# Kernel tuning notes

Measured on AMD Instinct MI355X. Metric: run time of the kernel, lower is better.

## Reference

```python
import jax, jax.numpy as jnp
import numpy as np

# ----- module constants (from init_kwargs) -----
N = 1024          # Np = [N, N]
NZ = 16           # number of slices (O.shape[3])
NA = 0.65         # objective NA
WL = 0.5          # wavelength (um)
PS = 6.5          # camera pixel size (um)
MAG = 20.0        # magnification
PS_EFF = PS / MAG
DZ = 10.0 * PS / MAG                 # slice spacing (code overwrites wl/na**2)
KAPPA = 2.0 * np.pi * DZ / WL        # imag part of self.k
K = np.complex64(1j * KAPPA)         # self.k as a complex scalar


def _grids():
    c = (np.arange(N) - N // 2) * PS_EFF
    xx, yy = np.meshgrid(c, c)                       # spatial grids
    f = (np.arange(N) - N // 2) / (PS_EFF * N)
    uxx, uyy = np.meshgrid(f, f)                     # frequency grids
    return xx, yy, uxx, uyy

_XX, _YY, _UXX, _UYY = _grids()
_URR = _UXX ** 2 + _UYY ** 2
_PC = (_URR < (NA / WL) ** 2).astype(np.float64)     # centered pupil


def _fresnel(dz):
    # genFrensel: band-limited angular-spectrum kernel, stored in fft order
    kz = np.sqrt(np.maximum(_PC * ((1.0 / WL) ** 2 - _URR), 0.0))
    kern = _PC * np.exp(1j * 2.0 * np.pi * dz * kz)
    return jnp.asarray(np.fft.fftshift(kern).astype(np.complex64))

PUPIL = jnp.asarray(np.fft.fftshift(_PC).astype(np.complex64))   # fft order
PROPKERN = _fresnel(DZ)
PROPKERN_FOCUS = _fresnel(-DZ * (NZ - 1) / 2.0)
XX = jnp.asarray(_XX, jnp.float32)
YY = jnp.asarray(_YY, jnp.float32)


def _prop(u, kern):
    # torch.fft / torch.ifft pair == unnormalized fft2 / normalized ifft2
    return jnp.fft.ifft2(jnp.fft.fft2(u) * kern)


def _plane_wave(na_illum):
    dfx = 1.0 / (PS_EFF * N)
    tilt = jnp.round((na_illum / WL) / dfx) * dfx    # snap tilt to freq grid
    phase = 2.0 * np.pi * (tilt[0] * XX + tilt[1] * YY)
    return jnp.exp(1j * phase)                        # complex64


def _ms_grad(O, intensity, na_illum):
    """Faithful translation of Multislice.grad. O: [N,N,NZ] complex64."""
    T = jnp.exp(K * O)                                # per-slice transmittance
    u = _plane_wave(na_illum)
    # forward multislice propagation
    for zz in range(NZ):
        u = T[..., zz] * u
        if zz < NZ - 1:
            u = _prop(u, PROPKERN)
    # refocus to stack center, apply pupil
    u_ref = _prop(u, PROPKERN_FOCUS)
    u_pup = _prop(u_ref, PUPIL)
    # amplitude-replacement residual
    abs_field = jnp.abs(u_pup)
    comp = jnp.sqrt(intensity) * u_pup / abs_field
    residual = u_pup - comp
    # back-propagate residual
    u_bp = _prop(residual, jnp.conj(PUPIL))
    u_bp = _prop(u_bp, jnp.conj(PROPKERN_FOCUS))
    # reverse slice loop accumulating per-slice gradient
    grads = [None] * NZ
    for zz in range(NZ - 1, -1, -1):
        grads[zz] = u_bp * jnp.conj(u) * jnp.conj(T[..., zz]) * np.conj(K)
        if zz > 0:
            u_bp = _prop(u_bp * jnp.conj(T[..., zz]), jnp.conj(PROPKERN))
            u = _prop(u, jnp.conj(PROPKERN))
            u = u / T[..., zz - 1]
    return jnp.stack(grads, axis=-1)                  # [N,N,NZ] complex


def setup_inputs() -> dict:
    key = jax.random.key(0)
    k1, k2, k3 = jax.random.split(key, 3)
    # small-valued object so exp(i*KAPPA*O) stays bounded (KAPPA ~ 40.8)
    x = jax.random.normal(k1, (N, N, 2, NZ), jnp.float32) * 0.01
    meas = jax.random.uniform(k2, (N, N), jnp.float32) + 0.1
    na_illum = jax.random.uniform(k3, (2,), jnp.float32) * 0.2
    alpha = jnp.full((1,), 0.01, jnp.float32)
    return {"x": x, "meas": meas, "na_illum": na_illum, "alpha": alpha}


def reference(x, meas, na_illum, alpha):
    # forward: x + step(x) = x - alpha * grad(x, meas, na_illum)
    O = x[..., 0, :] + 1j * x[..., 1, :]              # [N,N,NZ] complex64
    g = _ms_grad(O, meas, na_illum)
    out = O - alpha[0] * g
    return jnp.stack((out.real, out.imag), axis=2)    # back to [N,N,2,NZ]
```

## Files before the change

### kernel.cpp

```cpp
#include <hip/hip_runtime.h>
#include <math.h>


#define NN (1024*1024)
#define KAPPA 40.840704496667314f
#define TWO_PI_F 6.2831853071795865f
#define DFX_D 0.0030048076923076925
#define RRCUT 187177
#define F(i) ((i) + ((i)>>4))

#define JT 0
#define JT_WP 1
#define JRESID 3

__device__ __forceinline__ float2 cmulf(float2 a, float2 b){
    return make_float2(a.x*b.x - a.y*b.y, a.x*b.y + a.y*b.x);
}
__device__ __forceinline__ float2 cmulcj(float2 a, float2 b){
    return make_float2(a.x*b.x + a.y*b.y, a.y*b.x - a.x*b.y);
}
__device__ __forceinline__ float2 f2add(float2 a, float2 b){ return make_float2(a.x+b.x, a.y+b.y); }
__device__ __forceinline__ float2 f2sub(float2 a, float2 b){ return make_float2(a.x-b.x, a.y-b.y); }

__device__ __forceinline__ void fill_tw(float2* tw, int tid){
    #pragma unroll
    for (int k = tid; k < 512; k += 256){
        float s, c; sincosf(-(float)k * (TWO_PI_F/1024.0f), &s, &c);
        tw[k] = make_float2(c, s);
    }
}

__device__ __forceinline__ void dif_ph1(float2 r[8], const float2* tw, int lane){
    float2 a, d;
    #pragma unroll
    for (int k=0;k<4;++k){
        a=r[k]; d=f2sub(r[k],r[k+4]);
        r[k]=f2add(a,r[k+4]);
        r[k+4]=cmulf(d, tw[lane+128*k]);
    }
    float2 w20 = tw[lane<<1], w21 = tw[(lane+128)<<1];
    a=r[0]; d=f2sub(r[0],r[2]); r[0]=f2add(a,r[2]); r[2]=cmulf(d,w20);
    a=r[1]; d=f2sub(r[1],r[3]); r[1]=f2add(a,r[3]); r[3]=cmulf(d,w21);
    a=r[4]; d=f2sub(r[4],r[6]); r[4]=f2add(a,r[6]); r[6]=cmulf(d,w20);
    a=r[5]; d=f2sub(r[5],r[7]); r[5]=f2add(a,r[7]); r[7]=cmulf(d,w21);
    float2 w3 = tw[lane<<2];
    a=r[0]; d=f2sub(r[0],r[1]); r[0]=f2add(a,r[1]); r[1]=cmulf(d,w3);
    a=r[2]; d=f2sub(r[2],r[3]); r[2]=f2add(a,r[3]); r[3]=cmulf(d,w3);
    a=r[4]; d=f2sub(r[4],r[5]); r[4]=f2add(a,r[5]); r[5]=cmulf(d,w3);
    a=r[6]; d=f2sub(r[6],r[7]); r[6]=f2add(a,r[7]); r[7]=cmulf(d,w3);
}
__device__ __forceinline__ void dit_ph1(float2 r[8], const float2* tw, int lane){
    float2 a, b;
    float2 w3 = tw[lane<<2];
    a=r[0]; b=cmulcj(r[1],w3); r[0]=f2add(a,b); r[1]=f2sub(a,b);
    a=r[2]; b=cmulcj(r[3],w3); r[2]=f2add(a,b); r[3]=f2sub(a,b);
    a=r[4]; b=cmulcj(r[5],w3); r[4]=f2add(a,b); r[5]=f2sub(a,b);
    a=r[6]; b=cmulcj(r[7],w3); r[6]=f2add(a,b); r[7]=f2sub(a,b);
    float2 w20 = tw[lane<<1], w21 = tw[(lane+128)<<1];
    a=r[0]; b=cmulcj(r[2],w20); r[0]=f2add(a,b); r[2]=f2sub(a,b);
    a=r[1]; b=cmulcj(r[3],w21); r[1]=f2add(a,b); r[3]=f2sub(a,b);
    a=r[4]; b=cmulcj(r[6],w20); r[4]=f2add(a,b); r[6]=f2sub(a,b);
    a=r[5]; b=cmulcj(r[7],w21); r[5]=f2add(a,b); r[7]=f2sub(a,b);
    #pragma unroll
    for (int k=0;k<4;++k){
        a=r[k]; b=cmulcj(r[k+4], tw[lane+128*k]);
        r[k]=f2add(a,b); r[k+4]=f2sub(a,b);
    }
}
__device__ __forceinline__ void dif_ph2(float2 r[8], const float2* tw, int m0){
    float2 a, d;
    #pragma unroll
    for (int k=0;k<4;++k){
        a=r[k]; d=f2sub(r[k],r[k+4]);
        r[k]=f2add(a,r[k+4]);
        r[k+4]=cmulf(d, tw[(m0+16*k)<<3]);
    }
    float2 w40 = tw[m0<<4], w41 = tw[(m0+16)<<4];
    a=r[0]; d=f2sub(r[0],r[2]); r[0]=f2add(a,r[2]); r[2]=cmulf(d,w40);
    a=r[1]; d=f2sub(r[1],r[3]); r[1]=f2add(a,r[3]); r[3]=cmulf(d,w41);
    a=r[4]; d=f2sub(r[4],r[6]); r[4]=f2add(a,r[6]); r[6]=cmulf(d,w40);
    a=r[5]; d=f2sub(r[5],r[7]); r[5]=f2add(a,r[7]); r[7]=cmulf(d,w41);
    float2 w5 = tw[m0<<5];
    a=r[0]; d=f2sub(r[0],r[1]); r[0]=f2add(a,r[1]); r[1]=cmulf(d,w5);
    a=r[2]; d=f2sub(r[2],r[3]); r[2]=f2add(a,r[3]); r[3]=cmulf(d,w5);
    a=r[4]; d=f2sub(r[4],r[5]); r[4]=f2add(a,r[5]); r[5]=cmulf(d,w5);
    a=r[6]; d=f2sub(r[6],r[7]); r[6]=f2add(a,r[7]); r[7]=cmulf(d,w5);
}
__device__ __forceinline__ void dit_ph2(float2 r[8], const float2* tw, int m0){
    float2 a, b;
    float2 w5 = tw[m0<<5];
    a=r[0]; b=cmulcj(r[1],w5); r[0]=f2add(a,b); r[1]=f2sub(a,b);
    a=r[2]; b=cmulcj(r[3],w5); r[2]=f2add(a,b); r[3]=f2sub(a,b);
    a=r[4]; b=cmulcj(r[5],w5); r[4]=f2add(a,b); r[5]=f2sub(a,b);
    a=r[6]; b=cmulcj(r[7],w5); r[6]=f2add(a,b); r[7]=f2sub(a,b);
    float2 w40 = tw[m0<<4], w41 = tw[(m0+16)<<4];
    a=r[0]; b=cmulcj(r[2],w40); r[0]=f2add(a,b); r[2]=f2sub(a,b);
    a=r[1]; b=cmulcj(r[3],w41); r[1]=f2add(a,b); r[3]=f2sub(a,b);
    a=r[4]; b=cmulcj(r[6],w40); r[4]=f2add(a,b); r[6]=f2sub(a,b);
    a=r[5]; b=cmulcj(r[7],w41); r[5]=f2add(a,b); r[7]=f2sub(a,b);
    #pragma unroll
    for (int k=0;k<4;++k){
        a=r[k]; b=cmulcj(r[k+4], tw[(m0+16*k)<<3]);
        r[k]=f2add(a,b); r[k+4]=f2sub(a,b);
    }
}
__device__ __forceinline__ void dif_reg(float2 r[8]){
    const float C = 0.70710678118654752f;
    float2 a,d;
    a=r[0]; d=f2sub(r[0],r[4]); r[0]=f2add(a,r[4]); r[4]=d;
    a=r[1]; d=f2sub(r[1],r[5]); r[1]=f2add(a,r[5]); r[5]=make_float2(C*(d.x+d.y), C*(d.y-d.x));
    a=r[2]; d=f2sub(r[2],r[6]); r[2]=f2add(a,r[6]); r[6]=make_float2(d.y, -d.x);
    a=r[3]; d=f2sub(r[3],r[7]); r[3]=f2add(a,r[7]); r[7]=make_float2(C*(d.y-d.x), -C*(d.x+d.y));
    a=r[0]; r[0]=f2add(a,r[2]); r[2]=f2sub(a,r[2]);
    a=r[1]; d=f2sub(r[1],r[3]); r[1]=f2add(a,r[3]); r[3]=make_float2(d.y,-d.x);
    a=r[4]; r[4]=f2add(a,r[6]); r[6]=f2sub(a,r[6]);
    a=r[5]; d=f2sub(r[5],r[7]); r[5]=f2add(a,r[7]); r[7]=make_float2(d.y,-d.x);
    a=r[0]; r[0]=f2add(a,r[1]); r[1]=f2sub(a,r[1]);
    a=r[2]; r[2]=f2add(a,r[3]); r[3]=f2sub(a,r[3]);
    a=r[4]; r[4]=f2add(a,r[5]); r[5]=f2sub(a,r[5]);
    a=r[6]; r[6]=f2add(a,r[7]); r[7]=f2sub(a,r[7]);
}
__device__ __forceinline__ void dit_reg(float2 r[8]){
    const float C = 0.70710678118654752f;
    float2 a,b,t;
    a=r[0]; r[0]=f2add(a,r[1]); r[1]=f2sub(a,r[1]);
    a=r[2]; r[2]=f2add(a,r[3]); r[3]=f2sub(a,r[3]);
    a=r[4]; r[4]=f2add(a,r[5]); r[5]=f2sub(a,r[5]);
    a=r[6]; r[6]=f2add(a,r[7]); r[7]=f2sub(a,r[7]);
    a=r[0]; r[0]=f2add(a,r[2]); r[2]=f2sub(a,r[2]);
    a=r[1]; t=r[3]; b=make_float2(-t.y, t.x); r[1]=f2add(a,b); r[3]=f2sub(a,b);
    a=r[4]; r[4]=f2add(a,r[6]); r[6]=f2sub(a,r[6]);
    a=r[5]; t=r[7]; b=make_float2(-t.y, t.x); r[5]=f2add(a,b); r[7]=f2sub(a,b);
    a=r[0]; r[0]=f2add(a,r[4]); r[4]=f2sub(a,r[4]);
    a=r[1]; t=r[5]; b=make_float2(C*(t.x-t.y), C*(t.x+t.y)); r[1]=f2add(a,b); r[5]=f2sub(a,b);
    a=r[2]; t=r[6]; b=make_float2(-t.y, t.x); r[2]=f2add(a,b); r[6]=f2sub(a,b);
    a=r[3]; t=r[7]; b=make_float2(-C*(t.x+t.y), C*(t.x-t.y)); r[3]=f2add(a,b); r[7]=f2sub(a,b);
}

__device__ __forceinline__ void st128l(float2* L, int ro, int lane, const float2 r[8]){
    #pragma unroll
    for (int k=0;k<8;++k) L[F(ro + lane + 128*k)] = r[k];
}
__device__ __forceinline__ void ld128l(const float2* L, int ro, int lane, float2 r[8]){
    #pragma unroll
    for (int k=0;k<8;++k) r[k] = L[F(ro + lane + 128*k)];
}
__device__ __forceinline__ void st16l(float2* L, int ro, int lane, const float2 r[8]){
    int b = lane>>4, m0 = lane&15, q = ro + 128*b + m0;
    #pragma unroll
    for (int k=0;k<8;++k) L[F(q + 16*k)] = r[k];
}
__device__ __forceinline__ void ld16l(const float2* L, int ro, int lane, float2 r[8]){
    int b = lane>>4, m0 = lane&15, q = ro + 128*b + m0;
    #pragma unroll
    for (int k=0;k<8;++k) r[k] = L[F(q + 16*k)];
}
__device__ __forceinline__ void st8l(float2* L, int ro, int lane, const float2 r[8]){
    int q = ro + 8*lane;
    #pragma unroll
    for (int i=0;i<8;++i) L[F(q + i)] = r[i];
}
__device__ __forceinline__ void ldfold_dif(const float2* L, int ro, int lane,
                                           const float2* tw, float2 r[8]){
    int rr = lane>>1, sub = lane&1, q = ro + 16*rr;
    #pragma unroll
    for (int i=0;i<8;++i){
        float2 x = L[F(q + i)];
        float2 y = L[F(q + 8 + i)];
        r[i] = sub ? cmulf(f2sub(x,y), tw[i<<6]) : f2add(x,y);
    }
}
__device__ __forceinline__ void ldfold_dit(const float2* L, int ro, int lane,
                                           const float2* tw, float2 r[8]){
    int b = lane>>4, m0 = lane&15, m0s = m0&7;
    float2 w = tw[m0s<<6];
    int q = ro + 128*b + m0s;
    #pragma unroll
    for (int k=0;k<8;++k){
        float2 x = L[F(q + 16*k)];
        float2 y = L[F(q + 16*k + 8)];
        float2 bb = cmulcj(y, w);
        r[k] = (m0 < 8) ? f2add(x,bb) : f2sub(x,bb);
    }
}
__device__ __forceinline__ void load8g(const float2* src, int lane, float2 r[8]){
    const float4* s4 = (const float4*)src + lane*4;
    #pragma unroll
    for (int m=0;m<4;++m){
        float4 v = s4[m];
        r[2*m]   = make_float2(v.x, v.y);
        r[2*m+1] = make_float2(v.z, v.w);
    }
}
__device__ __forceinline__ void twrite2(const float2* L, int tid, float2* dst,
                                        int r0, float s){
    #pragma unroll
    for (int k=0;k<4;++k){
        int c = tid + (k<<8);
        float2 a0 = L[F(c)], a1 = L[F(1024+c)];
        ((float4*)(dst + ((size_t)c<<10) + r0))[0] =
            make_float4(a0.x*s, a0.y*s, a1.x*s, a1.y*s);
    }
}

__global__ void __launch_bounds__(256) k_head(float2* __restrict__ dst,
                                              const float2* __restrict__ T0,
                                              const float* __restrict__ nail){
    __shared__ float2 A[2176], B[2176], tw[512];
    const int tid = threadIdx.x;
    fill_tw(tw, tid);
    const int row = tid>>7, lane = tid&127, ro = row<<10, m0 = lane&15;
    const int r0 = blockIdx.x*2;
    const size_t gbase = ((size_t)(r0+row))<<10;
    float dfx = (float)DFX_D;
    float t0 = rintf(nail[0]*2.0f/dfx)*dfx;
    float t1 = rintf(nail[1]*2.0f/dfx)*dfx;
    float yv = (float)((r0+row) - 512) * 0.325f;
    float2 r[8];
    #pragma unroll
    for (int k=0;k<8;++k){
        int col = lane + 128*k;
        float2 tv = T0[gbase + col];
        float xv = (float)(col - 512) * 0.325f;
        float s0, c0; sincosf(TWO_PI_F*(t0*xv + t1*yv), &s0, &c0);
        r[k] = cmulf(make_float2(c0,s0), tv);
    }
    __syncthreads();
    dif_ph1(r, tw, lane);
    st128l(A, ro, lane, r); __syncthreads();
    ld16l(A, ro, lane, r); dif_ph2(r, tw, m0);
    st16l(B, ro, lane, r); __syncthreads();
    ldfold_dif(B, ro, lane, tw, r); dif_reg(r);
    st8l(A, ro, lane, r); __syncthreads();
    twrite2(A, tid, dst, r0, 1.0f);
}

__global__ void __launch_bounds__(256) k_pass2(
    const float2* __restrict__ srcA, float2* __restrict__ dstA,
    const float2* __restrict__ srcB, float2* __restrict__ dstB,
    double zscale, float sg)
{
    __shared__ float2 A[2176], B[2176], tw[512];
    const int tid = threadIdx.x;
    fill_tw(tw, tid);
    const int row = tid>>7, lane = tid&127, ro = row<<10, m0 = lane&15;
    int bid = blockIdx.x;
    const float2* src = srcA; float2* dst = dstA;
    if (srcB != nullptr && bid >= 512){ src = srcB; dst = dstB; bid -= 512; }
    const int r0 = bid*2;
    const int jrow = r0 + row;
    const float2* srcR = src + (((size_t)r0)<<10) + ro;
    float2 r[8];
    #pragma unroll
    for (int k=0;k<8;++k) r[k] = srcR[lane + 128*k];
    __syncthreads();
    dif_ph1(r, tw, lane);
    st128l(A, ro, lane, r); __syncthreads();
    ld16l(A, ro, lane, r); dif_ph2(r, tw, m0);
    st16l(B, ro, lane, r); __syncthreads();
    ldfold_dif(B, ro, lane, tw, r); dif_reg(r);
    {
        int bb = __brev((unsigned)jrow) >> 22;
        int rb = bb - (bb >= 512 ? 1024 : 0);
        int rb2 = rb*rb;
        #pragma unroll
        for (int i=0;i<8;++i){
            int aa = __brev((unsigned)(8*lane+i)) >> 22;
            int ra = aa - (aa >= 512 ? 1024 : 0);
            int rr = ra*ra + rb2;
            if (rr <= RRCUT){
                double urr = (double)rr * (DFX_D*DFX_D);
                double kz = sqrt(4.0 - urr);
                double t = zscale * kz;
                float fp = (float)(t - floor(t));
                float s, c; sincosf(TWO_PI_F*fp, &s, &c);
                r[i] = cmulf(r[i], make_float2(c, sg*s));
            } else {
                r[i] = make_float2(0.f, 0.f);
            }
        }
    }
    dit_reg(r);
    st8l(A, ro, lane, r); __syncthreads();
    ldfold_dit(A, ro, lane, tw, r); dit_ph2(r, tw, m0);
    st16l(B, ro, lane, r); __syncthreads();
    ld128l(B, ro, lane, r); dit_ph1(r, tw, lane);
    st128l(A, ro, lane, r); __syncthreads();
    twrite2(A, tid, dst, r0, 1.0f/1024.0f);
}

__global__ void __launch_bounds__(256) k_junc(
    const float2* __restrict__ src, float2* __restrict__ dst,
    const float2* __restrict__ Tz, float2* __restrict__ wp,
    const float* __restrict__ meas, int mode)
{
    __shared__ float2 A[2176], B[2176], tw[512];
    const int tid = threadIdx.x;
    fill_tw(tw, tid);
    const int row = tid>>7, lane = tid&127, ro = row<<10, m0 = lane&15;
    const int r0 = blockIdx.x*2;
    const size_t gbase = ((size_t)(r0+row))<<10;
    const float S = 1.0f/1024.0f;
    float2 r[8];
    load8g(src + (((size_t)r0)<<10) + ro, lane, r);
    float2 pre[8];
    if (mode == JT || mode == JT_WP){
        #pragma unroll
        for (int k=0;k<8;++k) pre[k] = Tz[gbase + lane + 128*k];
    } else if (mode == JRESID){
        #pragma unroll
        for (int k=0;k<8;++k) pre[k].x = meas[gbase + lane + 128*k];
    }
    dit_reg(r);
    st8l(A, ro, lane, r); __syncthreads();
    ldfold_dit(A, ro, lane, tw, r); dit_ph2(r, tw, m0);
    st16l(B, ro, lane, r); __syncthreads();
    ld128l(B, ro, lane, r); dit_ph1(r, tw, lane);
    #pragma unroll
    for (int k=0;k<8;++k){
        size_t g = gbase + lane + 128*k;
        float2 v = make_float2(S*r[k].x, S*r[k].y);
        if (mode == JT || mode == JT_WP){
            v = cmulf(v, pre[k]);
            if (mode == JT_WP) wp[g] = v;
        } else if (mode == JRESID){
            float m = pre[k].x;
            float aamp = fmaxf(sqrtf(v.x*v.x + v.y*v.y), 1e-30f);
            float f = 1.0f - sqrtf(m)/aamp;
            v.x *= f; v.y *= f;
        }
        r[k] = v;
    }
    dif_ph1(r, tw, lane);
    st128l(A, ro, lane, r); __syncthreads();
    ld16l(A, ro, lane, r); dif_ph2(r, tw, m0);
    st16l(B, ro, lane, r); __syncthreads();
    ldfold_dif(B, ro, lane, tw, r); dif_reg(r);
    st8l(A, ro, lane, r); __syncthreads();
    twrite2(A, tid, dst, r0, 1.0f);
}

__global__ void __launch_bounds__(256) k_rev(
    const float2* __restrict__ srcU, float2* __restrict__ dstU,
    const float2* __restrict__ srcB, float2* __restrict__ dstB,
    float2* __restrict__ Tz, int headU)
{
    __shared__ float2 A[2176], B[2176], tw[512];
    const int tid = threadIdx.x;
    fill_tw(tw, tid);
    const int row = tid>>7, lane = tid&127, ro = row<<10, m0 = lane&15;
    const int r0 = blockIdx.x*2;
    const size_t gbase = ((size_t)(r0+row))<<10;
    const float S = 1.0f/1024.0f;
    float2 u[8], Tg[8], bb[8], r[8];
    if (!headU){
        load8g(srcU + (((size_t)r0)<<10) + ro, lane, u);
    } else {
        const float2* srcR = srcU + (((size_t)r0)<<10) + ro;
        #pragma unroll
        for (int k=0;k<8;++k) u[k] = srcR[lane + 128*k];
    }
    #pragma unroll
    for (int k=0;k<8;++k) Tg[k] = Tz[gbase + lane + 128*k];
    load8g(srcB + (((size_t)r0)<<10) + ro, lane, bb);
    if (!headU){
        dit_reg(u);
        st8l(A, ro, lane, u); __syncthreads();
        ldfold_dit(A, ro, lane, tw, u); dit_ph2(u, tw, m0);
        st16l(B, ro, lane, u); __syncthreads();
        ld128l(B, ro, lane, u); dit_ph1(u, tw, lane);
        #pragma unroll
        for (int k=0;k<8;++k){ u[k].x *= S; u[k].y *= S; }
    } else {
        __syncthreads();
    }
    #pragma unroll
    for (int k=0;k<8;++k){
        if (headU) r[k] = u[k];
        else {
            float inv = 1.0f/(Tg[k].x*Tg[k].x + Tg[k].y*Tg[k].y);
            float2 wc = cmulcj(u[k], Tg[k]);
            r[k] = make_float2(wc.x*inv, wc.y*inv);
        }
    }
    dif_ph1(r, tw, lane);
    st128l(A, ro, lane, r); __syncthreads();
    ld16l(A, ro, lane, r); dif_ph2(r, tw, m0);
    st16l(B, ro, lane, r); __syncthreads();
    ldfold_dif(B, ro, lane, tw, r); dif_reg(r);
    st8l(A, ro, lane, r); __syncthreads();
    twrite2(A, tid, dstU, r0, 1.0f);
    dit_reg(bb);
    st8l(B, ro, lane, bb); __syncthreads();
    ldfold_dit(B, ro, lane, tw, r); dit_ph2(r, tw, m0);
    st16l(A, ro, lane, r); __syncthreads();
    ld128l(A, ro, lane, r); dit_ph1(r, tw, lane);
    #pragma unroll
    for (int k=0;k<8;++k){
        float2 b = make_float2(S*r[k].x, S*r[k].y);
        float2 q = headU ? cmulcj(cmulcj(b, u[k]), Tg[k]) : cmulcj(b, u[k]);
        Tz[gbase + lane + 128*k] = make_float2(KAPPA*q.y, -KAPPA*q.x);
        r[k] = cmulcj(b, Tg[k]);
    }
    dif_ph1(r, tw, lane);
    st128l(B, ro, lane, r); __syncthreads();
    ld16l(B, ro, lane, r); dif_ph2(r, tw, m0);
    st16l(A, ro, lane, r); __syncthreads();
    ldfold_dif(A, ro, lane, tw, r); dif_reg(r);
    st8l(B, ro, lane, r); __syncthreads();
    twrite2(B, tid, dstB, r0, 1.0f);
}

__global__ void __launch_bounds__(256) k_tail(
    const float2* __restrict__ srcU, const float2* __restrict__ srcB,
    float2* __restrict__ G0)
{
    __shared__ float2 A[2176], B[2176], tw[512];
    const int tid = threadIdx.x;
    fill_tw(tw, tid);
    const int row = tid>>7, lane = tid&127, ro = row<<10, m0 = lane&15;
    const int r0 = blockIdx.x*2;
    const size_t gbase = ((size_t)(r0+row))<<10;
    const float S = 1.0f/1024.0f;
    float2 u[8], r[8];
    load8g(srcU + (((size_t)r0)<<10) + ro, lane, u);
    load8g(srcB + (((size_t)r0)<<10) + ro, lane, r);
    dit_reg(u);
    st8l(A, ro, lane, u); __syncthreads();
    ldfold_dit(A, ro, lane, tw, u); dit_ph2(u, tw, m0);
    st16l(B, ro, lane, u); __syncthreads();
    ld128l(B, ro, lane, u); dit_ph1(u, tw, lane);
    dit_reg(r);
    st8l(A, ro, lane, r); __syncthreads();
    ldfold_dit(A, ro, lane, tw, r); dit_ph2(r, tw, m0);
    st16l(B, ro, lane, r); __syncthreads();
    ld128l(B, ro, lane, r); dit_ph1(r, tw, lane);
    #pragma unroll
    for (int k=0;k<8;++k){
        float2 b = make_float2(S*r[k].x, S*r[k].y);
        float2 w = make_float2(S*u[k].x, S*u[k].y);
        float2 q = cmulcj(b, w);
        G0[gbase + lane + 128*k] = make_float2(KAPPA*q.y, -KAPPA*q.x);
    }
}

__global__ void __launch_bounds__(256) k_T(const float4* __restrict__ x,
                                           float2* __restrict__ T){
    int idx = blockIdx.x*256 + threadIdx.x;
    int pp = idx >> 2;
    int q  = idx & 3;
    int p0 = pp*2;
    float4 vr0 = x[(size_t)p0*8 + q];
    float4 vi0 = x[(size_t)p0*8 + 4 + q];
    float4 vr1 = x[(size_t)(p0+1)*8 + q];
    float4 vi1 = x[(size_t)(p0+1)*8 + 4 + q];
    const float* fr0 = (const float*)&vr0;
    const float* fi0 = (const float*)&vi0;
    const float* fr1 = (const float*)&vr1;
    const float* fi1 = (const float*)&vi1;
    #pragma unroll
    for (int j=0;j<4;++j){
        int z = 4*q + j;
        float a0 = __expf(-KAPPA*fi0[j]);
        float s0, c0; __sincosf(KAPPA*fr0[j], &s0, &c0);
        float a1 = __expf(-KAPPA*fi1[j]);
        float s1, c1; __sincosf(KAPPA*fr1[j], &s1, &c1);
        ((float4*)(T + (size_t)z*NN + p0))[0] = make_float4(a0*c0, a0*s0, a1*c1, a1*s1);
    }
}

__global__ void __launch_bounds__(256) k_merge(const float4* __restrict__ x,
                                               const float2* __restrict__ G,
                                               const float* __restrict__ alpha,
                                               float4* __restrict__ out){
    int idx = blockIdx.x*256 + threadIdx.x;
    int p = idx >> 2, q = idx & 3;
    float al = alpha[0];
    float4 xr = x[(size_t)p*8 + q];
    float4 xi = x[(size_t)p*8 + 4 + q];
    float2 g[4];
    #pragma unroll
    for (int j=0;j<4;++j) g[j] = G[(size_t)(4*q+j)*NN + p];
    out[(size_t)p*8 + q]     = make_float4(xr.x - al*g[0].x, xr.y - al*g[1].x,
                                           xr.z - al*g[2].x, xr.w - al*g[3].x);
    out[(size_t)p*8 + 4 + q] = make_float4(xi.x - al*g[0].y, xi.y - al*g[1].y,
                                           xi.z - al*g[2].y, xi.w - al*g[3].y);
}

extern "C" void kernel_launch(void* const* d_in, const int* in_sizes, int n_in,
                              void* d_out, int out_size, void* d_ws, size_t ws_size,
                              hipStream_t stream)
{
    const float* x     = (const float*)d_in[0];
    const float* meas  = (const float*)d_in[1];
    const float* nail  = (const float*)d_in[2];
    const float* alpha = (const float*)d_in[3];

    if (ws_size < (size_t)21*NN*sizeof(float2)) return;

    float2* W   = (float2*)d_ws;
    float2* T   = W;
    float2* U0  = W + (size_t)16*NN;
    float2* TAB = W + (size_t)17*NN;
    float2* TBB = W + (size_t)18*NN;
    float2* TAU = W + (size_t)19*NN;
    float2* TBU = W + (size_t)20*NN;

    const double ZP = 3.25;
    const double ZF = -24.375;

    k_T <<<8192, 256, 0, stream>>>((const float4*)x, T);

    auto P2f = [&](double zs, float sg){
        k_pass2<<<512, 256, 0, stream>>>(TAB, TBB, nullptr, nullptr, zs, sg);
    };

    k_head<<<512, 256, 0, stream>>>(TAB, T, nail);
    P2f(ZP, 1.0f);
    for (int z = 1; z <= 14; ++z){
        k_junc<<<512, 256, 0, stream>>>(TBB, TAB, T + (size_t)z*NN, nullptr, nullptr, JT);
        P2f(ZP, 1.0f);
    }
    k_junc<<<512, 256, 0, stream>>>(TBB, TAB, T + (size_t)15*NN, U0, nullptr, JT_WP);
    P2f(ZF, 1.0f);
    k_junc<<<512, 256, 0, stream>>>(TBB, TAB, nullptr, nullptr, meas, JRESID);
    P2f(ZF, -1.0f);

    for (int zz = 15; zz >= 1; --zz){
        k_rev<<<512, 256, 0, stream>>>(zz == 15 ? U0 : TBU, TAU, TBB, TAB,
                                       T + (size_t)zz*NN, zz == 15 ? 1 : 0);
        k_pass2<<<1024, 256, 0, stream>>>(TAB, TBB, TAU, TBU, ZP, -1.0f);
    }
    k_tail<<<512, 256, 0, stream>>>(TBU, TBB, T);

    k_merge<<<16384, 256, 0, stream>>>((const float4*)x, T, alpha, (float4*)d_out);
}
```

Before: 1.421 ms.

## Switch row FFTs to radix-4 with 512 threads and fewer shared buffers

```diff
diff --git a/kernel.cpp b/kernel.cpp
--- a/kernel.cpp
+++ b/kernel.cpp
@@ -8,6 +8,7 @@
 #define DFX_D 0.0030048076923076925
 #define RRCUT 187177
 #define F(i) ((i) + ((i)>>4))
+#define NTW 768
 
 #define JT 0
 #define JT_WP 1
@@ -22,251 +23,197 @@
 __device__ __forceinline__ float2 f2add(float2 a, float2 b){ return make_float2(a.x+b.x, a.y+b.y); }
 __device__ __forceinline__ float2 f2sub(float2 a, float2 b){ return make_float2(a.x-b.x, a.y-b.y); }
 
-__device__ __forceinline__ void fill_tw(float2* tw, int tid){
-    #pragma unroll
-    for (int k = tid; k < 512; k += 256){
+__device__ __forceinline__ void fill_tw768(float2* tw, int tid){
+    for (int k = tid; k < NTW; k += 512){
         float s, c; sincosf(-(float)k * (TWO_PI_F/1024.0f), &s, &c);
         tw[k] = make_float2(c, s);
     }
 }
 
-__device__ __forceinline__ void dif_ph1(float2 r[8], const float2* tw, int lane){
-    float2 a, d;
-    #pragma unroll
-    for (int k=0;k<4;++k){
-        a=r[k]; d=f2sub(r[k],r[k+4]);
-        r[k]=f2add(a,r[k+4]);
-        r[k+4]=cmulf(d, tw[lane+128*k]);
-    }
-    float2 w20 = tw[lane<<1], w21 = tw[(lane+128)<<1];
-    a=r[0]; d=f2sub(r[0],r[2]); r[0]=f2add(a,r[2]); r[2]=cmulf(d,w20);
-    a=r[1]; d=f2sub(r[1],r[3]); r[1]=f2add(a,r[3]); r[3]=cmulf(d,w21);
-    a=r[4]; d=f2sub(r[4],r[6]); r[4]=f2add(a,r[6]); r[6]=cmulf(d,w20);
-    a=r[5]; d=f2sub(r[5],r[7]); r[5]=f2add(a,r[7]); r[7]=cmulf(d,w21);
-    float2 w3 = tw[lane<<2];
-    a=r[0]; d=f2sub(r[0],r[1]); r[0]=f2add(a,r[1]); r[1]=cmulf(d,w3);
-    a=r[2]; d=f2sub(r[2],r[3]); r[2]=f2add(a,r[3]); r[3]=cmulf(d,w3);
-    a=r[4]; d=f2sub(r[4],r[5]); r[4]=f2add(a,r[5]); r[5]=cmulf(d,w3);
-    a=r[6]; d=f2sub(r[6],r[7]); r[6]=f2add(a,r[7]); r[7]=cmulf(d,w3);
-}
-__device__ __forceinline__ void dit_ph1(float2 r[8], const float2* tw, int lane){
-    float2 a, b;
-    float2 w3 = tw[lane<<2];
-    a=r[0]; b=cmulcj(r[1],w3); r[0]=f2add(a,b); r[1]=f2sub(a,b);
-    a=r[2]; b=cmulcj(r[3],w3); r[2]=f2add(a,b); r[3]=f2sub(a,b);
-    a=r[4]; b=cmulcj(r[5],w3); r[4]=f2add(a,b); r[5]=f2sub(a,b);
-    a=r[6]; b=cmulcj(r[7],w3); r[6]=f2add(a,b); r[7]=f2sub(a,b);
-    float2 w20 = tw[lane<<1], w21 = tw[(lane+128)<<1];
-    a=r[0]; b=cmulcj(r[2],w20); r[0]=f2add(a,b); r[2]=f2sub(a,b);
-    a=r[1]; b=cmulcj(r[3],w21); r[1]=f2add(a,b); r[3]=f2sub(a,b);
-    a=r[4]; b=cmulcj(r[6],w20); r[4]=f2add(a,b); r[6]=f2sub(a,b);
-    a=r[5]; b=cmulcj(r[7],w21); r[5]=f2add(a,b); r[7]=f2sub(a,b);
-    #pragma unroll
-    for (int k=0;k<4;++k){
-        a=r[k]; b=cmulcj(r[k+4], tw[lane+128*k]);
-        r[k]=f2add(a,b); r[k+4]=f2sub(a,b);
-    }
-}
-__device__ __forceinline__ void dif_ph2(float2 r[8], const float2* tw, int m0){
-    float2 a, d;
-    #pragma unroll
-    for (int k=0;k<4;++k){
-        a=r[k]; d=f2sub(r[k],r[k+4]);
-        r[k]=f2add(a,r[k+4]);
-        r[k+4]=cmulf(d, tw[(m0+16*k)<<3]);
-    }
-    float2 w40 = tw[m0<<4], w41 = tw[(m0+16)<<4];
-    a=r[0]; d=f2sub(r[0],r[2]); r[0]=f2add(a,r[2]); r[2]=cmulf(d,w40);
-    a=r[1]; d=f2sub(r[1],r[3]); r[1]=f2add(a,r[3]); r[3]=cmulf(d,w41);
-    a=r[4]; d=f2sub(r[4],r[6]); r[4]=f2add(a,r[6]); r[6]=cmulf(d,w40);
-    a=r[5]; d=f2sub(r[5],r[7]); r[5]=f2add(a,r[7]); r[7]=cmulf(d,w41);
-    float2 w5 = tw[m0<<5];
-    a=r[0]; d=f2sub(r[0],r[1]); r[0]=f2add(a,r[1]); r[1]=cmulf(d,w5);
-    a=r[2]; d=f2sub(r[2],r[3]); r[2]=f2add(a,r[3]); r[3]=cmulf(d,w5);
-    a=r[4]; d=f2sub(r[4],r[5]); r[4]=f2add(a,r[5]); r[5]=cmulf(d,w5);
-    a=r[6]; d=f2sub(r[6],r[7]); r[6]=f2add(a,r[7]); r[7]=cmulf(d,w5);
-}
-__device__ __forceinline__ void dit_ph2(float2 r[8], const float2* tw, int m0){
-    float2 a, b;
-    float2 w5 = tw[m0<<5];
-    a=r[0]; b=cmulcj(r[1],w5); r[0]=f2add(a,b); r[1]=f2sub(a,b);
-    a=r[2]; b=cmulcj(r[3],w5); r[2]=f2add(a,b); r[3]=f2sub(a,b);
-    a=r[4]; b=cmulcj(r[5],w5); r[4]=f2add(a,b); r[5]=f2sub(a,b);
-    a=r[6]; b=cmulcj(r[7],w5); r[6]=f2add(a,b); r[7]=f2sub(a,b);
-    float2 w40 = tw[m0<<4], w41 = tw[(m0+16)<<4];
-    a=r[0]; b=cmulcj(r[2],w40); r[0]=f2add(a,b); r[2]=f2sub(a,b);
-    a=r[1]; b=cmulcj(r[3],w41); r[1]=f2add(a,b); r[3]=f2sub(a,b);
-    a=r[4]; b=cmulcj(r[6],w40); r[4]=f2add(a,b); r[6]=f2sub(a,b);
-    a=r[5]; b=cmulcj(r[7],w41); r[5]=f2add(a,b); r[7]=f2sub(a,b);
-    #pragma unroll
-    for (int k=0;k<4;++k){
-        a=r[k]; b=cmulcj(r[k+4], tw[(m0+16*k)<<3]);
-        r[k]=f2add(a,b); r[k+4]=f2sub(a,b);
-    }
-}
-__device__ __forceinline__ void dif_reg(float2 r[8]){
-    const float C = 0.70710678118654752f;
-    float2 a,d;
-    a=r[0]; d=f2sub(r[0],r[4]); r[0]=f2add(a,r[4]); r[4]=d;
-    a=r[1]; d=f2sub(r[1],r[5]); r[1]=f2add(a,r[5]); r[5]=make_float2(C*(d.x+d.y), C*(d.y-d.x));
-    a=r[2]; d=f2sub(r[2],r[6]); r[2]=f2add(a,r[6]); r[6]=make_float2(d.y, -d.x);
-    a=r[3]; d=f2sub(r[3],r[7]); r[3]=f2add(a,r[7]); r[7]=make_float2(C*(d.y-d.x), -C*(d.x+d.y));
-    a=r[0]; r[0]=f2add(a,r[2]); r[2]=f2sub(a,r[2]);
-    a=r[1]; d=f2sub(r[1],r[3]); r[1]=f2add(a,r[3]); r[3]=make_float2(d.y,-d.x);
-    a=r[4]; r[4]=f2add(a,r[6]); r[6]=f2sub(a,r[6]);
-    a=r[5]; d=f2sub(r[5],r[7]); r[5]=f2add(a,r[7]); r[7]=make_float2(d.y,-d.x);
-    a=r[0]; r[0]=f2add(a,r[1]); r[1]=f2sub(a,r[1]);
-    a=r[2]; r[2]=f2add(a,r[3]); r[3]=f2sub(a,r[3]);
-    a=r[4]; r[4]=f2add(a,r[5]); r[5]=f2sub(a,r[5]);
-    a=r[6]; r[6]=f2add(a,r[7]); r[7]=f2sub(a,r[7]);
-}
-__device__ __forceinline__ void dit_reg(float2 r[8]){
-    const float C = 0.70710678118654752f;
-    float2 a,b,t;
-    a=r[0]; r[0]=f2add(a,r[1]); r[1]=f2sub(a,r[1]);
-    a=r[2]; r[2]=f2add(a,r[3]); r[3]=f2sub(a,r[3]);
-    a=r[4]; r[4]=f2add(a,r[5]); r[5]=f2sub(a,r[5]);
-    a=r[6]; r[6]=f2add(a,r[7]); r[7]=f2sub(a,r[7]);
-    a=r[0]; r[0]=f2add(a,r[2]); r[2]=f2sub(a,r[2]);
-    a=r[1]; t=r[3]; b=make_float2(-t.y, t.x); r[1]=f2add(a,b); r[3]=f2sub(a,b);
-    a=r[4]; r[4]=f2add(a,r[6]); r[6]=f2sub(a,r[6]);
-    a=r[5]; t=r[7]; b=make_float2(-t.y, t.x); r[5]=f2add(a,b); r[7]=f2sub(a,b);
-    a=r[0]; r[0]=f2add(a,r[4]); r[4]=f2sub(a,r[4]);
-    a=r[1]; t=r[5]; b=make_float2(C*(t.x-t.y), C*(t.x+t.y)); r[1]=f2add(a,b); r[5]=f2sub(a,b);
-    a=r[2]; t=r[6]; b=make_float2(-t.y, t.x); r[2]=f2add(a,b); r[6]=f2sub(a,b);
-    a=r[3]; t=r[7]; b=make_float2(-C*(t.x+t.y), C*(t.x-t.y)); r[3]=f2add(a,b); r[7]=f2sub(a,b);
-}
-
-__device__ __forceinline__ void st128l(float2* L, int ro, int lane, const float2 r[8]){
-    #pragma unroll
-    for (int k=0;k<8;++k) L[F(ro + lane + 128*k)] = r[k];
-}
-__device__ __forceinline__ void ld128l(const float2* L, int ro, int lane, float2 r[8]){
-    #pragma unroll
-    for (int k=0;k<8;++k) r[k] = L[F(ro + lane + 128*k)];
-}
-__device__ __forceinline__ void st16l(float2* L, int ro, int lane, const float2 r[8]){
-    int b = lane>>4, m0 = lane&15, q = ro + 128*b + m0;
-    #pragma unroll
-    for (int k=0;k<8;++k) L[F(q + 16*k)] = r[k];
-}
-__device__ __forceinline__ void ld16l(const float2* L, int ro, int lane, float2 r[8]){
-    int b = lane>>4, m0 = lane&15, q = ro + 128*b + m0;
-    #pragma unroll
-    for (int k=0;k<8;++k) r[k] = L[F(q + 16*k)];
-}
-__device__ __forceinline__ void st8l(float2* L, int ro, int lane, const float2 r[8]){
-    int q = ro + 8*lane;
-    #pragma unroll
-    for (int i=0;i<8;++i) L[F(q + i)] = r[i];
-}
-__device__ __forceinline__ void ldfold_dif(const float2* L, int ro, int lane,
-                                           const float2* tw, float2 r[8]){
-    int rr = lane>>1, sub = lane&1, q = ro + 16*rr;
-    #pragma unroll
-    for (int i=0;i<8;++i){
-        float2 x = L[F(q + i)];
-        float2 y = L[F(q + 8 + i)];
-        r[i] = sub ? cmulf(f2sub(x,y), tw[i<<6]) : f2add(x,y);
-    }
-}
-__device__ __forceinline__ void ldfold_dit(const float2* L, int ro, int lane,
-                                           const float2* tw, float2 r[8]){
-    int b = lane>>4, m0 = lane&15, m0s = m0&7;
-    float2 w = tw[m0s<<6];
-    int q = ro + 128*b + m0s;
-    #pragma unroll
-    for (int k=0;k<8;++k){
-        float2 x = L[F(q + 16*k)];
-        float2 y = L[F(q + 16*k + 8)];
-        float2 bb = cmulcj(y, w);
-        r[k] = (m0 < 8) ? f2add(x,bb) : f2sub(x,bb);
-    }
-}
-__device__ __forceinline__ void load8g(const float2* src, int lane, float2 r[8]){
-    const float4* s4 = (const float4*)src + lane*4;
-    #pragma unroll
-    for (int m=0;m<4;++m){
-        float4 v = s4[m];
-        r[2*m]   = make_float2(v.x, v.y);
-        r[2*m+1] = make_float2(v.z, v.w);
-    }
-}
-__device__ __forceinline__ void twrite2(const float2* L, int tid, float2* dst,
-                                        int r0, float s){
-    #pragma unroll
-    for (int k=0;k<4;++k){
-        int c = tid + (k<<8);
+__device__ __forceinline__ void r4dif_tw(float2 r[4], const float2* tw, int e){
+    float2 A = f2add(r[0], r[2]), B = f2sub(r[0], r[2]);
+    float2 C = f2add(r[1], r[3]), D = f2sub(r[1], r[3]);
+    float2 jD = make_float2(-D.y, D.x);
+    r[0] = f2add(A, C);
+    r[1] = cmulf(f2sub(B, jD), tw[e]);
+    r[2] = cmulf(f2sub(A, C), tw[2*e]);
+    r[3] = cmulf(f2add(B, jD), tw[3*e]);
+}
+__device__ __forceinline__ void r4dif_nt(float2 r[4]){
+    float2 A = f2add(r[0], r[2]), B = f2sub(r[0], r[2]);
+    float2 C = f2add(r[1], r[3]), D = f2sub(r[1], r[3]);
+    float2 jD = make_float2(-D.y, D.x);
+    r[0] = f2add(A, C);
+    r[1] = f2sub(B, jD);
+    r[2] = f2sub(A, C);
+    r[3] = f2add(B, jD);
+}
+__device__ __forceinline__ void r4dit_tw(float2 r[4], const float2* tw, int e){
+    float2 t1 = cmulcj(r[1], tw[e]);
+    float2 t2 = cmulcj(r[2], tw[2*e]);
+    float2 t3 = cmulcj(r[3], tw[3*e]);
+    float2 E = f2add(r[0], t2), Fv = f2sub(r[0], t2);
+    float2 G = f2add(t1, t3),  H  = f2sub(t1, t3);
+    float2 jH = make_float2(-H.y, H.x);
+    r[0] = f2add(E, G);
+    r[1] = f2add(Fv, jH);
+    r[2] = f2sub(E, G);
+    r[3] = f2sub(Fv, jH);
+}
+__device__ __forceinline__ void r4dit_nt(float2 r[4]){
+    float2 E = f2add(r[0], r[2]), Fv = f2sub(r[0], r[2]);
+    float2 G = f2add(r[1], r[3]), H  = f2sub(r[1], r[3]);
+    float2 jH = make_float2(-H.y, H.x);
+    r[0] = f2add(E, G);
+    r[1] = f2add(Fv, jH);
+    r[2] = f2sub(E, G);
+    r[3] = f2sub(Fv, jH);
+}
+
+__device__ __forceinline__ void dif4(float2* L, const float2* tw, int ro, int lane,
+                                     float2 r[4]){
+    r4dif_tw(r, tw, lane);
+    #pragma unroll
+    for (int q=0;q<4;++q) L[F(ro + lane + 256*q)] = r[q];
+    __syncthreads();
+    const int b = lane>>6, m = lane&63, base2 = ro + 256*b + m;
+    #pragma unroll
+    for (int q=0;q<4;++q) r[q] = L[F(base2 + 64*q)];
+    r4dif_tw(r, tw, 4*m);
+    #pragma unroll
+    for (int q=0;q<4;++q) L[F(base2 + 64*q)] = r[q];
+    const int g = lane>>4, m3 = lane&15, base3 = ro + 64*g + m3;
+    #pragma unroll
+    for (int q=0;q<4;++q) r[q] = L[F(base3 + 16*q)];
+    r4dif_tw(r, tw, 16*m3);
+    #pragma unroll
+    for (int q=0;q<4;++q) L[F(base3 + 16*q)] = r[q];
+    const int h = lane>>2, m4 = lane&3, base4 = ro + 16*h + m4;
+    #pragma unroll
+    for (int q=0;q<4;++q) r[q] = L[F(base4 + 4*q)];
+    r4dif_tw(r, tw, 64*m4);
+    #pragma unroll
+    for (int q=0;q<4;++q) L[F(base4 + 4*q)] = r[q];
+    const int base5 = F(ro + 4*lane);
+    #pragma unroll
+    for (int q=0;q<4;++q) r[q] = L[base5 + q];
+    r4dif_nt(r);
+}
+__device__ __forceinline__ void dit4(float2* L, const float2* tw, int ro, int lane,
+                                     float2 r[4]){
+    r4dit_nt(r);
+    const int base5 = F(ro + 4*lane);
+    #pragma unroll
+    for (int q=0;q<4;++q) L[base5 + q] = r[q];
+    const int h = lane>>2, m4 = lane&3, base4 = ro + 16*h + m4;
+    #pragma unroll
+    for (int q=0;q<4;++q) r[q] = L[F(base4 + 4*q)];
+    r4dit_tw(r, tw, 64*m4);
+    #pragma unroll
+    for (int q=0;q<4;++q) L[F(base4 + 4*q)] = r[q];
+    const int g = lane>>4, m3 = lane&15, base3 = ro + 64*g + m3;
+    #pragma unroll
+    for (int q=0;q<4;++q) r[q] = L[F(base3 + 16*q)];
+    r4dit_tw(r, tw, 16*m3);
+    #pragma unroll
+    for (int q=0;q<4;++q) L[F(base3 + 16*q)] = r[q];
+    const int b = lane>>6, m = lane&63, base2 = ro + 256*b + m;
+    #pragma unroll
+    for (int q=0;q<4;++q) r[q] = L[F(base2 + 64*q)];
+    r4dit_tw(r, tw, 4*m);
+    #pragma unroll
+    for (int q=0;q<4;++q) L[F(base2 + 64*q)] = r[q];
+    __syncthreads();
+    #pragma unroll
+    for (int q=0;q<4;++q) r[q] = L[F(ro + lane + 256*q)];
+    r4dit_tw(r, tw, lane);
+}
+
+__device__ __forceinline__ void st_slot(float2* L, int ro, int lane, const float2 r[4]){
+    const int base = F(ro + 4*lane);
+    #pragma unroll
+    for (int q=0;q<4;++q) L[base + q] = r[q];
+}
+__device__ __forceinline__ void st_nat(float2* L, int ro, int lane, const float2 r[4]){
+    #pragma unroll
+    for (int m=0;m<4;++m) L[F(ro + lane + 256*m)] = r[m];
+}
+__device__ __forceinline__ void load4slot(const float2* src, int lane, float2 r[4]){
+    const float4* s4 = (const float4*)src + lane*2;
+    float4 v0 = s4[0], v1 = s4[1];
+    r[0] = make_float2(v0.x, v0.y); r[1] = make_float2(v0.z, v0.w);
+    r[2] = make_float2(v1.x, v1.y); r[3] = make_float2(v1.z, v1.w);
+}
+__device__ __forceinline__ void twr(const float2* L, int tid, float2* dst,
+                                    int r0, float s){
+    #pragma unroll
+    for (int k=0;k<2;++k){
+        int c = tid + (k<<9);
         float2 a0 = L[F(c)], a1 = L[F(1024+c)];
         ((float4*)(dst + ((size_t)c<<10) + r0))[0] =
             make_float4(a0.x*s, a0.y*s, a1.x*s, a1.y*s);
     }
 }
 
-__global__ void __launch_bounds__(256) k_head(float2* __restrict__ dst,
-                                              const float2* __restrict__ T0,
-                                              const float* __restrict__ nail){
-    __shared__ float2 A[2176], B[2176], tw[512];
+__global__ void __launch_bounds__(512,4) k_head(float2* __restrict__ dst,
+                                                const float2* __restrict__ T0,
+                                                const float* __restrict__ nail){
+    __shared__ float2 A[2176], tw[NTW];
     const int tid = threadIdx.x;
-    fill_tw(tw, tid);
-    const int row = tid>>7, lane = tid&127, ro = row<<10, m0 = lane&15;
+    fill_tw768(tw, tid);
+    const int row = tid>>8, lane = tid&255, ro = row<<10;
     const int r0 = blockIdx.x*2;
     const size_t gbase = ((size_t)(r0+row))<<10;
     float dfx = (float)DFX_D;
     float t0 = rintf(nail[0]*2.0f/dfx)*dfx;
     float t1 = rintf(nail[1]*2.0f/dfx)*dfx;
     float yv = (float)((r0+row) - 512) * 0.325f;
-    float2 r[8];
-    #pragma unroll
-    for (int k=0;k<8;++k){
-        int col = lane + 128*k;
+    float2 r[4];
+    #pragma unroll
+    for (int m=0;m<4;++m){
+        int col = lane + 256*m;
         float2 tv = T0[gbase + col];
         float xv = (float)(col - 512) * 0.325f;
         float s0, c0; sincosf(TWO_PI_F*(t0*xv + t1*yv), &s0, &c0);
-        r[k] = cmulf(make_float2(c0,s0), tv);
-    }
-    __syncthreads();
-    dif_ph1(r, tw, lane);
-    st128l(A, ro, lane, r); __syncthreads();
-    ld16l(A, ro, lane, r); dif_ph2(r, tw, m0);
-    st16l(B, ro, lane, r); __syncthreads();
-    ldfold_dif(B, ro, lane, tw, r); dif_reg(r);
-    st8l(A, ro, lane, r); __syncthreads();
-    twrite2(A, tid, dst, r0, 1.0f);
-}
-
-__global__ void __launch_bounds__(256) k_pass2(
+        r[m] = cmulf(make_float2(c0,s0), tv);
+    }
+    __syncthreads();
+    dif4(A, tw, ro, lane, r);
+    st_slot(A, ro, lane, r);
+    __syncthreads();
+    twr(A, tid, dst, r0, 1.0f);
+}
+
+__global__ void __launch_bounds__(512,4) k_pass2(
     const float2* __restrict__ srcA, float2* __restrict__ dstA,
     const float2* __restrict__ srcB, float2* __restrict__ dstB,
     double zscale, float sg)
 {
-    __shared__ float2 A[2176], B[2176], tw[512];
+    __shared__ float2 A[2176], tw[NTW];
     const int tid = threadIdx.x;
-    fill_tw(tw, tid);
-    const int row = tid>>7, lane = tid&127, ro = row<<10, m0 = lane&15;
+    fill_tw768(tw, tid);
+    const int row = tid>>8, lane = tid&255, ro = row<<10;
     int bid = blockIdx.x;
     const float2* src = srcA; float2* dst = dstA;
     if (srcB != nullptr && bid >= 512){ src = srcB; dst = dstB; bid -= 512; }
     const int r0 = bid*2;
     const int jrow = r0 + row;
     const float2* srcR = src + (((size_t)r0)<<10) + ro;
-    float2 r[8];
-    #pragma unroll
-    for (int k=0;k<8;++k) r[k] = srcR[lane + 128*k];
-    __syncthreads();
-    dif_ph1(r, tw, lane);
-    st128l(A, ro, lane, r); __syncthreads();
-    ld16l(A, ro, lane, r); dif_ph2(r, tw, m0);
-    st16l(B, ro, lane, r); __syncthreads();
-    ldfold_dif(B, ro, lane, tw, r); dif_reg(r);
+    float2 r[4];
+    #pragma unroll
+    for (int m=0;m<4;++m) r[m] = srcR[lane + 256*m];
+    __syncthreads();
+    dif4(A, tw, ro, lane, r);
     {
-        int bb = __brev((unsigned)jrow) >> 22;
-        int rb = bb - (bb >= 512 ? 1024 : 0);
+        int jr = ((jrow&3)<<8)|(((jrow>>2)&3)<<6)|(((jrow>>4)&3)<<4)
+               |(((jrow>>6)&3)<<2)|((jrow>>8)&3);
+        int rb = jr - (jr >= 512 ? 1024 : 0);
         int rb2 = rb*rb;
+        int lr = ((lane&3)<<6)|(((lane>>2)&3)<<4)|(((lane>>4)&3)<<2)|((lane>>6)&3);
         #pragma unroll
-        for (int i=0;i<8;++i){
-            int aa = __brev((unsigned)(8*lane+i)) >> 22;
-            int ra = aa - (aa >= 512 ? 1024 : 0);
+        for (int q=0;q<4;++q){
+            int fa = (q<<8) | lr;
+            int ra = fa - (fa >= 512 ? 1024 : 0);
             int rr = ra*ra + rb2;
             if (rr <= RRCUT){
                 double urr = (double)rr * (DFX_D*DFX_D);
@@ -274,173 +221,142 @@
                 double t = zscale * kz;
                 float fp = (float)(t - floor(t));
                 float s, c; sincosf(TWO_PI_F*fp, &s, &c);
-                r[i] = cmulf(r[i], make_float2(c, sg*s));
+                r[q] = cmulf(r[q], make_float2(c, sg*s));
             } else {
-                r[i] = make_float2(0.f, 0.f);
+                r[q] = make_float2(0.f, 0.f);
             }
         }
     }
-    dit_reg(r);
-    st8l(A, ro, lane, r); __syncthreads();
-    ldfold_dit(A, ro, lane, tw, r); dit_ph2(r, tw, m0);
-    st16l(B, ro, lane, r); __syncthreads();
-    ld128l(B, ro, lane, r); dit_ph1(r, tw, lane);
-    st128l(A, ro, lane, r); __syncthreads();
-    twrite2(A, tid, dst, r0, 1.0f/1024.0f);
-}
-
-__global__ void __launch_bounds__(256) k_junc(
+    dit4(A, tw, ro, lane, r);
+    st_nat(A, ro, lane, r);
+    __syncthreads();
+    twr(A, tid, dst, r0, 1.0f/1024.0f);
+}
+
+__global__ void __launch_bounds__(512,4) k_junc(
     const float2* __restrict__ src, float2* __restrict__ dst,
     const float2* __restrict__ Tz, float2* __restrict__ wp,
     const float* __restrict__ meas, int mode)
 {
-    __shared__ float2 A[2176], B[2176], tw[512];
+    __shared__ float2 A[2176], tw[NTW];
     const int tid = threadIdx.x;
-    fill_tw(tw, tid);
-    const int row = tid>>7, lane = tid&127, ro = row<<10, m0 = lane&15;
+    fill_tw768(tw, tid);
+    const int row = tid>>8, lane = tid&255, ro = row<<10;
     const int r0 = blockIdx.x*2;
     const size_t gbase = ((size_t)(r0+row))<<10;
     const float S = 1.0f/1024.0f;
-    float2 r[8];
-    load8g(src + (((size_t)r0)<<10) + ro, lane, r);
-    float2 pre[8];
+    float2 r[4];
+    load4slot(src + (((size_t)r0)<<10) + ro, lane, r);
+    float2 pre[4];
     if (mode == JT || mode == JT_WP){
         #pragma unroll
-        for (int k=0;k<8;++k) pre[k] = Tz[gbase + lane + 128*k];
+        for (int m=0;m<4;++m) pre[m] = Tz[gbase + lane + 256*m];
     } else if (mode == JRESID){
         #pragma unroll
-        for (int k=0;k<8;++k) pre[k].x = meas[gbase + lane + 128*k];
-    }
-    dit_reg(r);
-    st8l(A, ro, lane, r); __syncthreads();
-    ldfold_dit(A, ro, lane, tw, r); dit_ph2(r, tw, m0);
-    st16l(B, ro, lane, r); __syncthreads();
-    ld128l(B, ro, lane, r); dit_ph1(r, tw, lane);
-    #pragma unroll
-    for (int k=0;k<8;++k){
-        size_t g = gbase + lane + 128*k;
-        float2 v = make_float2(S*r[k].x, S*r[k].y);
+        for (int m=0;m<4;++m) pre[m].x = meas[gbase + lane + 256*m];
+    }
+    __syncthreads();
+    dit4(A, tw, ro, lane, r);
+    #pragma unroll
+    for (int m=0;m<4;++m){
+        size_t g = gbase + lane + 256*m;
+        float2 v = make_float2(S*r[m].x, S*r[m].y);
         if (mode == JT || mode == JT_WP){
-            v = cmulf(v, pre[k]);
+            v = cmulf(v, pre[m]);
             if (mode == JT_WP) wp[g] = v;
         } else if (mode == JRESID){
-            float m = pre[k].x;
+            float mm = pre[m].x;
             float aamp = fmaxf(sqrtf(v.x*v.x + v.y*v.y), 1e-30f);
-            float f = 1.0f - sqrtf(m)/aamp;
+            float f = 1.0f - sqrtf(mm)/aamp;
             v.x *= f; v.y *= f;
         }
-        r[k] = v;
-    }
-    dif_ph1(r, tw, lane);
-    st128l(A, ro, lane, r); __syncthreads();
-    ld16l(A, ro, lane, r); dif_ph2(r, tw, m0);
-    st16l(B, ro, lane, r); __syncthreads();
-    ldfold_dif(B, ro, lane, tw, r); dif_reg(r);
-    st8l(A, ro, lane, r); __syncthreads();
-    twrite2(A, tid, dst, r0, 1.0f);
-}
-
-__global__ void __launch_bounds__(256) k_rev(
+        r[m] = v;
+    }
+    dif4(A, tw, ro, lane, r);
+    st_slot(A, ro, lane, r);
+    __syncthreads();
+    twr(A, tid, dst, r0, 1.0f);
+}
+
+__global__ void __launch_bounds__(512,4) k_rev(
     const float2* __restrict__ srcU, float2* __restrict__ dstU,
     const float2* __restrict__ srcB, float2* __restrict__ dstB,
     float2* __restrict__ Tz, int headU)
 {
-    __shared__ float2 A[2176], B[2176], tw[512];
+    __shared__ float2 A[2176], Bb[2176], tw[NTW];
     const int tid = threadIdx.x;
-    fill_tw(tw, tid);
-    const int row = tid>>7, lane = tid&127, ro = row<<10, m0 = lane&15;
+    fill_tw768(tw, tid);
+    const int row = tid>>8, lane = tid&255, ro = row<<10;
     const int r0 = blockIdx.x*2;
     const size_t gbase = ((size_t)(r0+row))<<10;
     const float S = 1.0f/1024.0f;
-    float2 u[8], Tg[8], bb[8], r[8];
+    float2 u[4], Tg[4], bb[4], r[4];
     if (!headU){
-        load8g(srcU + (((size_t)r0)<<10) + ro, lane, u);
+        load4slot(srcU + (((size_t)r0)<<10) + ro, lane, u);
     } else {
-        const float2* srcR = srcU + (((size_t)r0)<<10) + ro;
+        const float2* sR = srcU + (((size_t)r0)<<10) + ro;
         #pragma unroll
-        for (int k=0;k<8;++k) u[k] = srcR[lane + 128*k];
-    }
-    #pragma unroll
-    for (int k=0;k<8;++k) Tg[k] = Tz[gbase + lane + 128*k];
-    load8g(srcB + (((size_t)r0)<<10) + ro, lane, bb);
+        for (int m=0;m<4;++m) u[m] = sR[lane + 256*m];
+    }
+    #pragma unroll
+    for (int m=0;m<4;++m) Tg[m] = Tz[gbase + lane + 256*m];
+    load4slot(srcB + (((size_t)r0)<<10) + ro, lane, bb);
+    __syncthreads();
     if (!headU){
-        dit_reg(u);
-        st8l(A, ro, lane, u); __syncthreads();
-        ldfold_dit(A, ro, lane, tw, u); dit_ph2(u, tw, m0);
-        st16l(B, ro, lane, u); __syncthreads();
-        ld128l(B, ro, lane, u); dit_ph1(u, tw, lane);
+        dit4(A, tw, ro, lane, u);
         #pragma unroll
-        for (int k=0;k<8;++k){ u[k].x *= S; u[k].y *= S; }
-    } else {
-        __syncthreads();
-    }
-    #pragma unroll
-    for (int k=0;k<8;++k){
-        if (headU) r[k] = u[k];
+        for (int m=0;m<4;++m){ u[m].x *= S; u[m].y *= S; }
+    }
+    #pragma unroll
+    for (int m=0;m<4;++m){
+        if (headU) r[m] = u[m];
         else {
-            float inv = 1.0f/(Tg[k].x*Tg[k].x + Tg[k].y*Tg[k].y);
-            float2 wc = cmulcj(u[k], Tg[k]);
-            r[k] = make_float2(wc.x*inv, wc.y*inv);
+            float inv = 1.0f/(Tg[m].x*Tg[m].x + Tg[m].y*Tg[m].y);
+            float2 wc = cmulcj(u[m], Tg[m]);
+            r[m] = make_float2(wc.x*inv, wc.y*inv);
         }
     }
-    dif_ph1(r, tw, lane);
-    st128l(A, ro, lane, r); __syncthreads();
-    ld16l(A, ro, lane, r); dif_ph2(r, tw, m0);
-    st16l(B, ro, lane, r); __syncthreads();
-    ldfold_dif(B, ro, lane, tw, r); dif_reg(r);
-    st8l(A, ro, lane, r); __syncthreads();
-    twrite2(A, tid, dstU, r0, 1.0f);
-    dit_reg(bb);
-    st8l(B, ro, lane, bb); __syncthreads();
-    ldfold_dit(B, ro, lane, tw, r); dit_ph2(r, tw, m0);
-    st16l(A, ro, lane, r); __syncthreads();
-    ld128l(A, ro, lane, r); dit_ph1(r, tw, lane);
-    #pragma unroll
-    for (int k=0;k<8;++k){
-        float2 b = make_float2(S*r[k].x, S*r[k].y);
-        float2 q = headU ? cmulcj(cmulcj(b, u[k]), Tg[k]) : cmulcj(b, u[k]);
-        Tz[gbase + lane + 128*k] = make_float2(KAPPA*q.y, -KAPPA*q.x);
-        r[k] = cmulcj(b, Tg[k]);
-    }
-    dif_ph1(r, tw, lane);
-    st128l(B, ro, lane, r); __syncthreads();
-    ld16l(B, ro, lane, r); dif_ph2(r, tw, m0);
-    st16l(A, ro, lane, r); __syncthreads();
-    ldfold_dif(A, ro, lane, tw, r); dif_reg(r);
-    st8l(B, ro, lane, r); __syncthreads();
-    twrite2(B, tid, dstB, r0, 1.0f);
-}
-
-__global__ void __launch_bounds__(256) k_tail(
+    dif4(A, tw, ro, lane, r);
+    st_slot(A, ro, lane, r);
+    __syncthreads();
+    twr(A, tid, dstU, r0, 1.0f);
+    dit4(Bb, tw, ro, lane, bb);
+    #pragma unroll
+    for (int m=0;m<4;++m){
+        float2 b2 = make_float2(S*bb[m].x, S*bb[m].y);
+        float2 q2 = headU ? cmulcj(cmulcj(b2, u[m]), Tg[m]) : cmulcj(b2, u[m]);
+        Tz[gbase + lane + 256*m] = make_float2(KAPPA*q2.y, -KAPPA*q2.x);
+        r[m] = cmulcj(b2, Tg[m]);
+    }
+    dif4(Bb, tw, ro, lane, r);
+    st_slot(Bb, ro, lane, r);
+    __syncthreads();
+    twr(Bb, tid, dstB, r0, 1.0f);
+}
+
+__global__ void __launch_bounds__(512,4) k_tail(
     const float2* __restrict__ srcU, const float2* __restrict__ srcB,
     float2* __restrict__ G0)
 {
-    __shared__ float2 A[2176], B[2176], tw[512];
+    __shared__ float2 A[2176], Bb[2176], tw[NTW];
     const int tid = threadIdx.x;
-    fill_tw(tw, tid);
-    const int row = tid>>7, lane = tid&127, ro = row<<10, m0 = lane&15;
+    fill_tw768(tw, tid);
+    const int row = tid>>8, lane = tid&255, ro = row<<10;
     const int r0 = blockIdx.x*2;
     const size_t gbase = ((size_t)(r0+row))<<10;
     const float S = 1.0f/1024.0f;
-    float2 u[8], r[8];
-    load8g(srcU + (((size_t)r0)<<10) + ro, lane, u);
-    load8g(srcB + (((size_t)r0)<<10) + ro, lane, r);
-    dit_reg(u);
-    st8l(A, ro, lane, u); __syncthreads();
-    ldfold_dit(A, ro, lane, tw, u); dit_ph2(u, tw, m0);
-    st16l(B, ro, lane, u); __syncthreads();
-    ld128l(B, ro, lane, u); dit_ph1(u, tw, lane);
-    dit_reg(r);
-    st8l(A, ro, lane, r); __syncthreads();
-    ldfold_dit(A, ro, lane, tw, r); dit_ph2(r, tw, m0);
-    st16l(B, ro, lane, r); __syncthreads();
-    ld128l(B, ro, lane, r); dit_ph1(r, tw, lane);
-    #pragma unroll
-    for (int k=0;k<8;++k){
-        float2 b = make_float2(S*r[k].x, S*r[k].y);
-        float2 w = make_float2(S*u[k].x, S*u[k].y);
-        float2 q = cmulcj(b, w);
-        G0[gbase + lane + 128*k] = make_float2(KAPPA*q.y, -KAPPA*q.x);
+    float2 u[4], r[4];
+    load4slot(srcU + (((size_t)r0)<<10) + ro, lane, u);
+    load4slot(srcB + (((size_t)r0)<<10) + ro, lane, r);
+    __syncthreads();
+    dit4(A,  tw, ro, lane, u);
+    dit4(Bb, tw, ro, lane, r);
+    #pragma unroll
+    for (int m=0;m<4;++m){
+        float2 b2 = make_float2(S*r[m].x, S*r[m].y);
+        float2 w2 = make_float2(S*u[m].x, S*u[m].y);
+        float2 q2 = cmulcj(b2, w2);
+        G0[gbase + lane + 256*m] = make_float2(KAPPA*q2.y, -KAPPA*q2.x);
     }
 }
 
@@ -512,26 +428,26 @@
     k_T <<<8192, 256, 0, stream>>>((const float4*)x, T);
 
     auto P2f = [&](double zs, float sg){
-        k_pass2<<<512, 256, 0, stream>>>(TAB, TBB, nullptr, nullptr, zs, sg);
+        k_pass2<<<512, 512, 0, stream>>>(TAB, TBB, nullptr, nullptr, zs, sg);
     };
 
-    k_head<<<512, 256, 0, stream>>>(TAB, T, nail);
+    k_head<<<512, 512, 0, stream>>>(TAB, T, nail);
     P2f(ZP, 1.0f);
     for (int z = 1; z <= 14; ++z){
-        k_junc<<<512, 256, 0, stream>>>(TBB, TAB, T + (size_t)z*NN, nullptr, nullptr, JT);
+        k_junc<<<512, 512, 0, stream>>>(TBB, TAB, T + (size_t)z*NN, nullptr, nullptr, JT);
         P2f(ZP, 1.0f);
     }
-    k_junc<<<512, 256, 0, stream>>>(TBB, TAB, T + (size_t)15*NN, U0, nullptr, JT_WP);
+    k_junc<<<512, 512, 0, stream>>>(TBB, TAB, T + (size_t)15*NN, U0, nullptr, JT_WP);
     P2f(ZF, 1.0f);
-    k_junc<<<512, 256, 0, stream>>>(TBB, TAB, nullptr, nullptr, meas, JRESID);
+    k_junc<<<512, 512, 0, stream>>>(TBB, TAB, nullptr, nullptr, meas, JRESID);
     P2f(ZF, -1.0f);
 
     for (int zz = 15; zz >= 1; --zz){
-        k_rev<<<512, 256, 0, stream>>>(zz == 15 ? U0 : TBU, TAU, TBB, TAB,
+        k_rev<<<512, 512, 0, stream>>>(zz == 15 ? U0 : TBU, TAU, TBB, TAB,
                                        T + (size_t)zz*NN, zz == 15 ? 1 : 0);
-        k_pass2<<<1024, 256, 0, stream>>>(TAB, TBB, TAU, TBU, ZP, -1.0f);
-    }
-    k_tail<<<512, 256, 0, stream>>>(TBU, TBB, T);
+        k_pass2<<<1024, 512, 0, stream>>>(TAB, TBB, TAU, TBU, ZP, -1.0f);
+    }
+    k_tail<<<512, 512, 0, stream>>>(TBU, TBB, T);
 
     k_merge<<<16384, 256, 0, stream>>>((const float4*)x, T, alpha, (float4*)d_out);
 }
```

Result: no change. 1.403 ms (-1.3%).
